# Kernel optimization log

Measured on AMD Instinct MI355X. Metric: run time of the kernel, lower is better.

Reference implementation:

```python
import jax, jax.numpy as jnp
import numpy as np

N, E, T = 6144, 98304, 32
D_IN, D, D_FF, H, OUT = 128, 256, 256, 4, 2
DH = D // H
EPS = 1e-5


def setup_inputs() -> dict:
    key = jax.random.key(0)
    ks = jax.random.split(key, 24)
    s = 0.05
    inp = {
        "x": jax.random.normal(ks[0], (N, D_IN), jnp.float32),
        "edge_index": jax.random.randint(ks[1], (2, E), 0, N, jnp.int64 if jax.config.jax_enable_x64 else jnp.int32),
        "timesteps": jnp.sort(jax.random.randint(ks[2], (N,), 0, T)),
        "lin_l_w": jax.random.normal(ks[3], (D, D_IN), jnp.float32) * s,
        "lin_l_b": jnp.zeros((D,), jnp.float32),
        "lin_r_w": jax.random.normal(ks[4], (D, D_IN), jnp.float32) * s,
        "bn_gamma": jnp.ones((D,), jnp.float32),
        "bn_beta": jnp.zeros((D,), jnp.float32),
        "in_proj_w": jax.random.normal(ks[5], (2, 3 * D, D), jnp.float32) * s,
        "in_proj_b": jnp.zeros((2, 3 * D), jnp.float32),
        "out_w": jax.random.normal(ks[6], (2, D, D), jnp.float32) * s,
        "out_b": jnp.zeros((2, D), jnp.float32),
        "ff1_w": jax.random.normal(ks[7], (2, D_FF, D), jnp.float32) * s,
        "ff1_b": jnp.zeros((2, D_FF), jnp.float32),
        "ff2_w": jax.random.normal(ks[8], (2, D, D_FF), jnp.float32) * s,
        "ff2_b": jnp.zeros((2, D), jnp.float32),
        "ln1_g": jnp.ones((2, D), jnp.float32),
        "ln1_b": jnp.zeros((2, D), jnp.float32),
        "ln2_g": jnp.ones((2, D), jnp.float32),
        "ln2_b": jnp.zeros((2, D), jnp.float32),
        "cls_w": jax.random.normal(ks[9], (OUT, D), jnp.float32) * s,
        "cls_b": jnp.zeros((OUT,), jnp.float32),
    }
    return inp


def _layernorm(h, g, b):
    mu = jnp.mean(h, -1, keepdims=True)
    v = jnp.var(h, -1, keepdims=True)
    return (h - mu) * jax.lax.rsqrt(v + EPS) * g + b


def _forward(x, edge_index, timesteps, lin_l_w, lin_l_b, lin_r_w, bn_gamma, bn_beta,
             in_proj_w, in_proj_b, out_w, out_b, ff1_w, ff1_b, ff2_w, ff2_b,
             ln1_g, ln1_b, ln2_g, ln2_b, cls_w, cls_b):
    # SAGEConv (mean aggregation): out = lin_l(mean_{j->i} x_j) + lin_r(x_i)
    src, dst = edge_index[0], edge_index[1]
    agg = jax.ops.segment_sum(x[src], dst, num_segments=N)
    cnt = jax.ops.segment_sum(jnp.ones((E,), x.dtype), dst, num_segments=N)
    agg = agg / jnp.maximum(cnt, 1.0)[:, None]
    h = agg @ lin_l_w.T + lin_l_b + x @ lin_r_w.T

    # BatchNorm1d (training batch stats) + ReLU
    mu = jnp.mean(h, 0)
    var = jnp.var(h, 0)
    h = (h - mu) * jax.lax.rsqrt(var + EPS) * bn_gamma + bn_beta
    h = jax.nn.relu(h)

    # Per-timestep transformer == full attention with block-diagonal mask
    mask = timesteps[:, None] == timesteps[None, :]  # [N, N]
    neg = jnp.finfo(h.dtype).min

    for l in range(2):
        # self-attention (post-norm TransformerEncoderLayer)
        qkv = h @ in_proj_w[l].T + in_proj_b[l]             # [N, 3D]
        q, k, v = jnp.split(qkv, 3, axis=-1)
        q = q.reshape(N, H, DH).transpose(1, 0, 2)          # [H, N, DH]
        k = k.reshape(N, H, DH).transpose(1, 0, 2)
        v = v.reshape(N, H, DH).transpose(1, 0, 2)
        scores = jnp.einsum('hnd,hmd->hnm', q, k) / jnp.sqrt(jnp.asarray(DH, h.dtype))
        scores = jnp.where(mask[None], scores, neg)
        attn = jax.nn.softmax(scores, axis=-1)
        o = jnp.einsum('hnm,hmd->hnd', attn, v).transpose(1, 0, 2).reshape(N, D)
        o = o @ out_w[l].T + out_b[l]
        h = _layernorm(h + o, ln1_g[l], ln1_b[l])
        # FFN
        f = jax.nn.relu(h @ ff1_w[l].T + ff1_b[l]) @ ff2_w[l].T + ff2_b[l]
        h = _layernorm(h + f, ln2_g[l], ln2_b[l])

    return h @ cls_w.T + cls_b  # [N, OUT]


def reference(x, edge_index, timesteps, lin_l_w, lin_l_b, lin_r_w, bn_gamma, bn_beta,
              in_proj_w, in_proj_b, out_w, out_b, ff1_w, ff1_b, ff2_w, ff2_b,
              ln1_g, ln1_b, ln2_g, ln2_b, cls_w, cls_b):
    return _forward(x, edge_index, timesteps, lin_l_w, lin_l_b, lin_r_w, bn_gamma, bn_beta,
                    in_proj_w, in_proj_b, out_w, out_b, ff1_w, ff1_b, ff2_w, ff2_b,
                    ln1_g, ln1_b, ln2_g, ln2_b, cls_w, cls_b)
```

## Files before the change

kernel.cpp:

```cpp
#include <hip/hip_runtime.h>

#define NN   6144
#define EE   98304
#define DIN  128
#define DD   256
#define TT   32
#define NH   4
#define ATTN_Z 6
#define WROWS 3328

typedef __attribute__((ext_vector_type(8))) short short8;
typedef __attribute__((ext_vector_type(4))) float f32x4;
typedef unsigned short u16;

__device__ __forceinline__ float bf2f(u16 u) {
    return __uint_as_float(((unsigned)u) << 16);
}
__device__ __forceinline__ u16 f2bf(float f) {
    unsigned u = __float_as_uint(f);
    return (u16)((u + 0x7fffu + ((u >> 16) & 1u)) >> 16);
}
__device__ __forceinline__ unsigned pk2(float a, float b) {
    return (unsigned)f2bf(a) | ((unsigned)f2bf(b) << 16);
}
__device__ __forceinline__ float bnrelu(float v, float s, float q, float g, float b) {
    float mu = s * (1.0f / NN);
    float var = q * (1.0f / NN) - mu * mu;
    return fmaxf((v - mu) * rsqrtf(var + 1e-5f) * g + b, 0.0f);
}

__global__ void aml_hist_k(const int* __restrict__ ei, int* __restrict__ deg) {
    int e = blockIdx.x * 256 + threadIdx.x;
    if (e < EE) atomicAdd(&deg[ei[EE + e]], 1);
}

__global__ void aml_scan_k(const int* __restrict__ deg, int* __restrict__ rowptr,
                           int* __restrict__ cursor) {
    int t = threadIdx.x;
    int base = t * 24;
    int loc[24];
    int s = 0;
    #pragma unroll
    for (int j = 0; j < 24; ++j) { loc[j] = s; s += deg[base + j]; }
    __shared__ int part[256];
    part[t] = s;
    __syncthreads();
    for (int o = 1; o < 256; o <<= 1) {
        int v = (t >= o) ? part[t - o] : 0;
        __syncthreads();
        part[t] += v;
        __syncthreads();
    }
    int off = (t > 0) ? part[t - 1] : 0;
    #pragma unroll
    for (int j = 0; j < 24; ++j) {
        rowptr[base + j] = off + loc[j];
        cursor[base + j] = off + loc[j];
    }
    if (t == 255) rowptr[NN] = part[255];
}

__global__ void aml_scatter2_k(const int* __restrict__ ei, int* __restrict__ cursor,
                               int* __restrict__ eid) {
    int e = blockIdx.x * 256 + threadIdx.x;
    if (e >= EE) return;
    int slot = atomicAdd(&cursor[ei[EE + e]], 1);
    eid[slot] = ei[e];
}

__global__ void aml_gather_k(const float* __restrict__ x, const int* __restrict__ rowptr,
                             const int* __restrict__ eid, u16* __restrict__ ac) {
    int node = blockIdx.x * 4 + (threadIdx.x >> 6);
    int lane = threadIdx.x & 63;
    int p0 = rowptr[node], p1 = rowptr[node + 1];
    float ax = 0.f, ay = 0.f;
    int j = p0;
    for (; j + 1 < p1; j += 2) {
        int s0 = eid[j], s1 = eid[j + 1];
        float2 v0 = *(const float2*)(x + (size_t)s0 * DIN + lane * 2);
        float2 v1 = *(const float2*)(x + (size_t)s1 * DIN + lane * 2);
        ax += v0.x + v1.x; ay += v0.y + v1.y;
    }
    if (j < p1) {
        float2 v = *(const float2*)(x + (size_t)eid[j] * DIN + lane * 2);
        ax += v.x; ay += v.y;
    }
    float inv = 1.0f / fmaxf((float)(p1 - p0), 1.0f);
    float2 xr = *(const float2*)(x + (size_t)node * DIN + lane * 2);
    *(unsigned*)(ac + (size_t)node * DD + lane * 2) = pk2(ax * inv, ay * inv);
    *(unsigned*)(ac + (size_t)node * DD + DIN + lane * 2) = pk2(xr.x, xr.y);
}

__global__ void aml_prep_k(const float* __restrict__ lin_l_w, const float* __restrict__ lin_r_w,
                           const float* __restrict__ inp_w, const float* __restrict__ out_w,
                           const float* __restrict__ ff1_w, const float* __restrict__ ff2_w,
                           const int* __restrict__ ts, u16* __restrict__ wb,
                           int* __restrict__ offs) {
    int r = blockIdx.x;
    if (r == WROWS) {
        int t = threadIdx.x;
        if (t <= TT) {
            int lo = 0, hi = NN;
            while (lo < hi) { int mid = (lo + hi) >> 1; if (ts[mid] < t) lo = mid + 1; else hi = mid; }
            offs[t] = lo;
        }
        return;
    }
    int k = threadIdx.x;
    float v;
    if (r < 256) {
        v = (k < DIN) ? lin_l_w[r * DIN + k] : lin_r_w[r * DIN + (k - DIN)];
    } else {
        int r2 = r - 256;
        int l = r2 / 1536, r3 = r2 % 1536;
        const float* src; int rr;
        if (r3 < 768)       { src = inp_w + (size_t)l * 768 * DD; rr = r3; }
        else if (r3 < 1024) { src = out_w + (size_t)l * DD * DD;  rr = r3 - 768; }
        else if (r3 < 1280) { src = ff1_w + (size_t)l * DD * DD;  rr = r3 - 1024; }
        else                { src = ff2_w + (size_t)l * DD * DD;  rr = r3 - 1280; }
        v = src[(size_t)rr * DD + k];
    }
    wb[(size_t)r * DD + k] = f2bf(v);
}

template <int RELU, int AF32, int CF32, int BNSTAT, int BNAPPLY>
__global__ __launch_bounds__(256)
void aml_gemm_k(const void* __restrict__ A, const u16* __restrict__ Wb,
                const float* __restrict__ bias, void* __restrict__ C, int M,
                float* __restrict__ stats, const float* __restrict__ bng,
                const float* __restrict__ bnb, float* __restrict__ h2) {
    __shared__ __align__(16) unsigned char lds[65536];
    const int t = threadIdx.x;
    const int brow = blockIdx.x * 64;
    const int bcol = blockIdx.y * 64;

    const u16* srcW = Wb + (size_t)bcol * 256;
    #pragma unroll
    for (int p = 0; p < 8; ++p) {
        int c = t + p * 256;
        int row = c >> 5;
        int colb = (c & 31) * 16;
        int dst = row * 512 + (colb ^ ((row & 7) << 4));
        if (AF32) {
            const float* sA = (const float*)A + (size_t)(brow + row) * 256 + (c & 31) * 8;
            float4 a0 = *(const float4*)sA;
            float4 a1 = *(const float4*)(sA + 4);
            if (BNAPPLY) {
                int d0 = (c & 31) * 8;
                float4 s0 = *(const float4*)(stats + d0);
                float4 s1 = *(const float4*)(stats + d0 + 4);
                float4 q0 = *(const float4*)(stats + DD + d0);
                float4 q1 = *(const float4*)(stats + DD + d0 + 4);
                float4 g0 = *(const float4*)(bng + d0), g1 = *(const float4*)(bng + d0 + 4);
                float4 b0 = *(const float4*)(bnb + d0), b1 = *(const float4*)(bnb + d0 + 4);
                a0.x = bnrelu(a0.x, s0.x, q0.x, g0.x, b0.x);
                a0.y = bnrelu(a0.y, s0.y, q0.y, g0.y, b0.y);
                a0.z = bnrelu(a0.z, s0.z, q0.z, g0.z, b0.z);
                a0.w = bnrelu(a0.w, s0.w, q0.w, g0.w, b0.w);
                a1.x = bnrelu(a1.x, s1.x, q1.x, g1.x, b1.x);
                a1.y = bnrelu(a1.y, s1.y, q1.y, g1.y, b1.y);
                a1.z = bnrelu(a1.z, s1.z, q1.z, g1.z, b1.z);
                a1.w = bnrelu(a1.w, s1.w, q1.w, g1.w, b1.w);
                if (blockIdx.y == 0) {
                    float* hp = h2 + (size_t)(brow + row) * 256 + d0;
                    *(float4*)hp = a0;
                    *(float4*)(hp + 4) = a1;
                }
            }
            uint4 pa = { pk2(a0.x, a0.y), pk2(a0.z, a0.w), pk2(a1.x, a1.y), pk2(a1.z, a1.w) };
            *(uint4*)(lds + dst) = pa;
        } else {
            const u16* sA = (const u16*)A + (size_t)(brow + row) * 256 + (c & 31) * 8;
            *(uint4*)(lds + dst) = *(const uint4*)sA;
        }
        *(uint4*)(lds + 32768 + dst) = *(const uint4*)(srcW + (size_t)row * 256 + (c & 31) * 8);
    }
    __syncthreads();

    const int wave = t >> 6, lane = t & 63;
    const int lrow = lane & 15, lk = lane >> 4;
    const int arow = wave * 16 + lrow;
    f32x4 acc[4] = {};
    #pragma unroll
    for (int ks = 0; ks < 8; ++ks) {
        int kbyte = ks * 64 + lk * 16;
        short8 af = *(const short8*)(lds + arow * 512 + (kbyte ^ ((arow & 7) << 4)));
        #pragma unroll
        for (int ct = 0; ct < 4; ++ct) {
            int wrow = ct * 16 + lrow;
            short8 bf = *(const short8*)(lds + 32768 + wrow * 512 + (kbyte ^ ((wrow & 7) << 4)));
            acc[ct] = __builtin_amdgcn_mfma_f32_16x16x32_bf16(af, bf, acc[ct], 0, 0, 0);
        }
    }

    #pragma unroll
    for (int ct = 0; ct < 4; ++ct) {
        int col = bcol + ct * 16 + lrow;
        float bv = bias[col];
        float s = 0.f, q = 0.f;
        #pragma unroll
        for (int r = 0; r < 4; ++r) {
            int grow = brow + wave * 16 + lk * 4 + r;
            float v = acc[ct][r] + bv;
            if (RELU) v = fmaxf(v, 0.0f);
            if (CF32) ((float*)C)[(size_t)grow * M + col] = v;
            else      ((u16*)C)[(size_t)grow * M + col] = f2bf(v);
            if (BNSTAT) { s += v; q += v * v; }
        }
        if (BNSTAT) {
            s += __shfl_xor(s, 16); s += __shfl_xor(s, 32);
            q += __shfl_xor(q, 16); q += __shfl_xor(q, 32);
            if (lk == 0) {
                atomicAdd(&stats[col], s);
                atomicAdd(&stats[DD + col], q);
            }
        }
    }
}

template <int CLS>
__global__ __launch_bounds__(256)
void aml_mega_k(const u16* __restrict__ A, const u16* __restrict__ Wb,
                const float* __restrict__ bias, float* __restrict__ h,
                const float* __restrict__ g, const float* __restrict__ bv,
                const float* __restrict__ cls_w, const float* __restrict__ cls_b,
                float* __restrict__ out) {
    __shared__ __align__(16) unsigned char Al[8192];
    __shared__ __align__(16) unsigned char Wl[32768];
    __shared__ float reds[4][16], redq[4][16];
    __shared__ float redc[2][4][16];
    const int t = threadIdx.x;
    const int brow = blockIdx.x * 16;
    const int wave = t >> 6, lane = t & 63;
    const int lrow = lane & 15, lk = lane >> 4;
    const int wcol = wave * 64;

    #pragma unroll
    for (int p = 0; p < 2; ++p) {
        int c = t + p * 256;
        int row = c >> 5;
        int c8 = c & 31;
        const u16* sA = A + (size_t)(brow + row) * 256 + c8 * 8;
        *(uint4*)(Al + row * 512 + ((c8 * 16) ^ ((row & 7) << 4))) = *(const uint4*)sA;
    }

    short8 af[8];
    f32x4 acc[4] = {};
    for (int kc = 0; kc < 4; ++kc) {
        if (kc) __syncthreads();
        #pragma unroll
        for (int p = 0; p < 8; ++p) {
            int c = t + p * 256;
            int row = c >> 3, sub = c & 7;
            *(uint4*)(Wl + row * 128 + ((sub * 16) ^ ((row & 7) << 4))) =
                *(const uint4*)(Wb + (size_t)row * 256 + kc * 64 + sub * 8);
        }
        __syncthreads();
        if (kc == 0) {
            #pragma unroll
            for (int ks = 0; ks < 8; ++ks) {
                int kbyte = ks * 64 + lk * 16;
                af[ks] = *(const short8*)(Al + lrow * 512 + (kbyte ^ ((lrow & 7) << 4)));
            }
        }
        #pragma unroll
        for (int s = 0; s < 2; ++s) {
            int kb = s * 64 + lk * 16;
            #pragma unroll
            for (int ct = 0; ct < 4; ++ct) {
                int wrow = wcol + ct * 16 + lrow;
                short8 bf = *(const short8*)(Wl + wrow * 128 + (kb ^ ((wrow & 7) << 4)));
                acc[ct] = __builtin_amdgcn_mfma_f32_16x16x32_bf16(af[kc * 2 + s], bf, acc[ct], 0, 0, 0);
            }
        }
    }

    float s4[4] = {}, q4[4] = {};
    #pragma unroll
    for (int ct = 0; ct < 4; ++ct) {
        int col = wcol + ct * 16 + lrow;
        float bvv = bias[col];
        #pragma unroll
        for (int r = 0; r < 4; ++r) {
            int grow = brow + lk * 4 + r;
            float v = acc[ct][r] + bvv + h[(size_t)grow * DD + col];
            acc[ct][r] = v;
            s4[r] += v; q4[r] += v * v;
        }
    }
    #pragma unroll
    for (int off = 1; off < 16; off <<= 1) {
        #pragma unroll
        for (int r = 0; r < 4; ++r) {
            s4[r] += __shfl_xor(s4[r], off);
            q4[r] += __shfl_xor(q4[r], off);
        }
    }
    if (lrow == 0) {
        #pragma unroll
        for (int r = 0; r < 4; ++r) {
            reds[wave][lk * 4 + r] = s4[r];
            redq[wave][lk * 4 + r] = q4[r];
        }
    }
    __syncthreads();
    float mu[4], iv[4];
    #pragma unroll
    for (int r = 0; r < 4; ++r) {
        int rr = lk * 4 + r;
        float S = reds[0][rr] + reds[1][rr] + reds[2][rr] + reds[3][rr];
        float Q = redq[0][rr] + redq[1][rr] + redq[2][rr] + redq[3][rr];
        mu[r] = S * (1.0f / DD);
        iv[r] = rsqrtf(Q * (1.0f / DD) - mu[r] * mu[r] + 1e-5f);
    }
    float c0[4] = {}, c1[4] = {};
    #pragma unroll
    for (int ct = 0; ct < 4; ++ct) {
        int col = wcol + ct * 16 + lrow;
        float gv = g[col], bb = bv[col];
        float w0 = CLS ? cls_w[col] : 0.f;
        float w1 = CLS ? cls_w[DD + col] : 0.f;
        #pragma unroll
        for (int r = 0; r < 4; ++r) {
            int grow = brow + lk * 4 + r;
            float v = (acc[ct][r] - mu[r]) * iv[r] * gv + bb;
            h[(size_t)grow * DD + col] = v;
            if (CLS) { c0[r] += v * w0; c1[r] += v * w1; }
        }
    }
    if (CLS) {
        #pragma unroll
        for (int off = 1; off < 16; off <<= 1) {
            #pragma unroll
            for (int r = 0; r < 4; ++r) {
                c0[r] += __shfl_xor(c0[r], off);
                c1[r] += __shfl_xor(c1[r], off);
            }
        }
        if (lrow == 0) {
            #pragma unroll
            for (int r = 0; r < 4; ++r) {
                redc[0][wave][lk * 4 + r] = c0[r];
                redc[1][wave][lk * 4 + r] = c1[r];
            }
        }
        __syncthreads();
        if (wave == 0 && lrow == 0) {
            float cb0 = cls_b[0], cb1 = cls_b[1];
            #pragma unroll
            for (int r = 0; r < 4; ++r) {
                int rr = lk * 4 + r;
                float o0 = redc[0][0][rr] + redc[0][1][rr] + redc[0][2][rr] + redc[0][3][rr];
                float o1 = redc[1][0][rr] + redc[1][1][rr] + redc[1][2][rr] + redc[1][3][rr];
                out[(brow + rr) * 2]     = o0 + cb0;
                out[(brow + rr) * 2 + 1] = o1 + cb1;
            }
        }
    }
}

__global__ __launch_bounds__(256)
void aml_attn_k(const u16* __restrict__ qkv, const int* __restrict__ offs,
                u16* __restrict__ o) {
    int tb = blockIdx.x, head = blockIdx.y, z = blockIdx.z;
    int start = offs[tb], end = offs[tb + 1];
    int S = end - start;
    if (S <= z * 64) return;
    int t = threadIdx.x, wave = t >> 6, lane = t & 63;
    int lq = lane & 15, lk = lane >> 4;
    int qoff = head * 64;

    __shared__ __align__(16) unsigned char Kl[8192];
    __shared__ __align__(16) unsigned char Vt[8192];
    __shared__ __align__(16) unsigned char Pl[4][2048];
    __shared__ float Ol[4][16][65];

    int qi = start + z * 64 + wave * 16 + lq;
    int qic = min(qi, end - 1);
    const u16* qp = qkv + (size_t)qic * 768 + qoff + lk * 8;
    short8 qf[2];
    qf[0] = *(const short8*)qp;
    qf[1] = *(const short8*)(qp + 32);

    float m = -1e30f, l = 0.f;
    f32x4 acc[4] = {};

    int ntile = (S + 63) >> 6;
    for (int tile = 0; tile < ntile; ++tile) {
        int jcnt = S - tile * 64; if (jcnt > 64) jcnt = 64;
        {
            int j = t >> 2, d0 = (t & 3) * 16;
            unsigned char* krow = Kl + j * 128;
            if (j < jcnt) {
                const u16* kp = qkv + (size_t)(start + tile * 64 + j) * 768 + 256 + qoff + d0;
                *(uint4*)(krow + ((d0 * 2) ^ ((j & 7) << 4))) = *(const uint4*)kp;
                *(uint4*)(krow + ((d0 * 2 + 16) ^ ((j & 7) << 4))) = *(const uint4*)(kp + 8);
                const u16* vp = kp + 256;
                #pragma unroll
                for (int i = 0; i < 16; ++i) {
                    int d = d0 + i;
                    *(u16*)(Vt + d * 128 + ((j * 2) ^ ((d & 7) << 4))) = vp[i];
                }
            } else {
                uint4 zz = { 0, 0, 0, 0 };
                *(uint4*)(krow + ((d0 * 2) ^ ((j & 7) << 4))) = zz;
                *(uint4*)(krow + ((d0 * 2 + 16) ^ ((j & 7) << 4))) = zz;
                #pragma unroll
                for (int i = 0; i < 16; ++i) {
                    int d = d0 + i;
                    *(u16*)(Vt + d * 128 + ((j * 2) ^ ((d & 7) << 4))) = 0;
                }
            }
        }
        __syncthreads();

        f32x4 sv[4];
        #pragma unroll
        for (int kt = 0; kt < 4; ++kt) {
            int kr = kt * 16 + lq;
            f32x4 s = {};
            #pragma unroll
            for (int ks = 0; ks < 2; ++ks) {
                short8 kf = *(const short8*)(Kl + kr * 128 + ((ks * 64 + lk * 16) ^ ((kr & 7) << 4)));
                s = __builtin_amdgcn_mfma_f32_16x16x32_bf16(kf, qf[ks], s, 0, 0, 0);
            }
            sv[kt] = s;
        }
        float pm = -1e30f;
        #pragma unroll
        for (int kt = 0; kt < 4; ++kt) {
            #pragma unroll
            for (int r = 0; r < 4; ++r) {
                int kk = tile * 64 + kt * 16 + lk * 4 + r;
                float s = (kk < S) ? sv[kt][r] * 0.125f : -1e30f;
                sv[kt][r] = s;
                pm = fmaxf(pm, s);
            }
        }
        pm = fmaxf(pm, __shfl_xor(pm, 16));
        pm = fmaxf(pm, __shfl_xor(pm, 32));
        float mn = fmaxf(m, pm);
        float corr = __expf(m - mn);
        m = mn;
        float ps = 0.f;
        #pragma unroll
        for (int kt = 0; kt < 4; ++kt) {
            #pragma unroll
            for (int r = 0; r < 4; ++r) {
                float p = __expf(sv[kt][r] - mn);
                sv[kt][r] = p;
                ps += p;
            }
            uint2 w = { pk2(sv[kt][0], sv[kt][1]), pk2(sv[kt][2], sv[kt][3]) };
            *(uint2*)(Pl[wave] + lq * 128 + ((kt * 32 + lk * 8) ^ ((lq & 7) << 4))) = w;
        }
        ps += __shfl_xor(ps, 16);
        ps += __shfl_xor(ps, 32);
        l = l * corr + ps;
        #pragma unroll
        for (int dt = 0; dt < 4; ++dt) {
            #pragma unroll
            for (int r = 0; r < 4; ++r) acc[dt][r] *= corr;
        }
        #pragma unroll
        for (int ks = 0; ks < 2; ++ks) {
            short8 pf = *(const short8*)(Pl[wave] + lq * 128 + ((ks * 64 + lk * 16) ^ ((lq & 7) << 4)));
            #pragma unroll
            for (int dt = 0; dt < 4; ++dt) {
                int dr = dt * 16 + lq;
                short8 vf = *(const short8*)(Vt + dr * 128 + ((ks * 64 + lk * 16) ^ ((dr & 7) << 4)));
                acc[dt] = __builtin_amdgcn_mfma_f32_16x16x32_bf16(vf, pf, acc[dt], 0, 0, 0);
            }
        }
        __syncthreads();
    }

    float linv = 1.0f / l;
    #pragma unroll
    for (int dt = 0; dt < 4; ++dt) {
        #pragma unroll
        for (int r = 0; r < 4; ++r)
            Ol[wave][lq][dt * 16 + lk * 4 + r] = acc[dt][r] * linv;
    }
    int q2 = lane >> 2, c2 = lane & 3;
    int qg = start + z * 64 + wave * 16 + q2;
    if (qg < end) {
        u16* op = o + (size_t)qg * DD + qoff + c2 * 16;
        const float* sp = &Ol[wave][q2][c2 * 16];
        #pragma unroll
        for (int i = 0; i < 8; ++i)
            ((unsigned*)op)[i] = pk2(sp[2 * i], sp[2 * i + 1]);
    }
}

extern "C" void kernel_launch(void* const* d_in, const int* in_sizes, int n_in,
                              void* d_out, int out_size, void* d_ws, size_t ws_size,
                              hipStream_t stream) {
    const float* x       = (const float*)d_in[0];
    const int*   ei      = (const int*)d_in[1];
    const int*   ts      = (const int*)d_in[2];
    const float* lin_l_w = (const float*)d_in[3];
    const float* lin_l_b = (const float*)d_in[4];
    const float* lin_r_w = (const float*)d_in[5];
    const float* bn_g    = (const float*)d_in[6];
    const float* bn_b    = (const float*)d_in[7];
    const float* inp_w   = (const float*)d_in[8];
    const float* inp_b   = (const float*)d_in[9];
    const float* out_w   = (const float*)d_in[10];
    const float* out_b   = (const float*)d_in[11];
    const float* ff1_w   = (const float*)d_in[12];
    const float* ff1_b   = (const float*)d_in[13];
    const float* ff2_w   = (const float*)d_in[14];
    const float* ff2_b   = (const float*)d_in[15];
    const float* ln1_g   = (const float*)d_in[16];
    const float* ln1_b   = (const float*)d_in[17];
    const float* ln2_g   = (const float*)d_in[18];
    const float* ln2_b   = (const float*)d_in[19];
    const float* cls_w   = (const float*)d_in[20];
    const float* cls_b   = (const float*)d_in[21];

    float* ws     = (float*)d_ws;
    float* stats  = ws;
    int*   deg    = (int*)(stats + 512);
    int*   rowptr = deg + NN;
    int*   cursor = rowptr + NN + 4;
    int*   eid    = cursor + NN;
    int*   offs   = eid + EE;
    u16*   wb     = (u16*)(offs + 64);
    float* h      = (float*)(wb + (size_t)WROWS * 256);
    float* h2     = h + (size_t)NN * DD;
    u16*   qkv    = (u16*)(h2 + (size_t)NN * DD);
    u16*   t1     = qkv + (size_t)NN * 768;
    u16*   ac     = qkv;

    const u16* wb_cat = wb;
    const u16* wb_inp[2] = { wb + (size_t)(256) * 256,        wb + (size_t)(256 + 1536) * 256 };
    const u16* wb_out[2] = { wb + (size_t)(256 + 768) * 256,  wb + (size_t)(256 + 1536 + 768) * 256 };
    const u16* wb_ff1[2] = { wb + (size_t)(256 + 1024) * 256, wb + (size_t)(256 + 1536 + 1024) * 256 };
    const u16* wb_ff2[2] = { wb + (size_t)(256 + 1280) * 256, wb + (size_t)(256 + 1536 + 1280) * 256 };

    hipMemsetAsync(stats, 0, 512 * sizeof(float) + NN * sizeof(int), stream);

    aml_hist_k<<<EE / 256, 256, 0, stream>>>(ei, deg);
    aml_scan_k<<<1, 256, 0, stream>>>(deg, rowptr, cursor);
    aml_scatter2_k<<<EE / 256, 256, 0, stream>>>(ei, cursor, eid);
    aml_gather_k<<<NN / 4, 256, 0, stream>>>(x, rowptr, eid, ac);
    aml_prep_k<<<WROWS + 1, 256, 0, stream>>>(lin_l_w, lin_r_w, inp_w, out_w, ff1_w, ff2_w,
                                              ts, wb, offs);
    aml_gemm_k<0, 0, 1, 1, 0><<<dim3(NN / 64, 4), 256, 0, stream>>>(
        ac, wb_cat, lin_l_b, h, DD, stats, nullptr, nullptr, nullptr);

    for (int l = 0; l < 2; ++l) {
        if (l == 0)
            aml_gemm_k<0, 1, 0, 0, 1><<<dim3(NN / 64, 12), 256, 0, stream>>>(
                h, wb_inp[0], inp_b, qkv, 768, stats, bn_g, bn_b, h2);
        else
            aml_gemm_k<0, 1, 0, 0, 0><<<dim3(NN / 64, 12), 256, 0, stream>>>(
                h2, wb_inp[1], inp_b + 768, qkv, 768, nullptr, nullptr, nullptr, nullptr);
        aml_attn_k<<<dim3(TT, NH, ATTN_Z), 256, 0, stream>>>(qkv, offs, t1);
        aml_mega_k<0><<<NN / 16, 256, 0, stream>>>(t1, wb_out[l], out_b + (size_t)l * DD, h2,
                                                   ln1_g + (size_t)l * DD, ln1_b + (size_t)l * DD,
                                                   nullptr, nullptr, nullptr);
        aml_gemm_k<1, 1, 0, 0, 0><<<dim3(NN / 64, 4), 256, 0, stream>>>(
            h2, wb_ff1[l], ff1_b + (size_t)l * DD, t1, DD, nullptr, nullptr, nullptr, nullptr);
        if (l == 0)
            aml_mega_k<0><<<NN / 16, 256, 0, stream>>>(t1, wb_ff2[0], ff2_b, h2,
                                                       ln2_g, ln2_b, nullptr, nullptr, nullptr);
        else
            aml_mega_k<1><<<NN / 16, 256, 0, stream>>>(t1, wb_ff2[1], ff2_b + DD, h2,
                                                       ln2_g + DD, ln2_b + DD,
                                                       cls_w, cls_b, (float*)d_out);
    }
}
```

Before: 162.5 us.

## Use bf16 activation copies and 128-column GEMM tiles reusing A fragments

Mega kernels now write a bf16 copy of the residual stream alongside the fp32 one, and the following GEMMs read that bf16 copy instead of converting fp32 on load. The SAGE GEMM writes bf16 output, and the BN+ReLU step is applied while loading that bf16 input. Each GEMM block now covers two 64-column weight tiles, keeping A fragments in registers and reloading only W, which halves the grid and the redundant A loads. The memset is replaced by a small zero kernel. The cost is extra bf16 stores, extra syncs inside the GEMM, and an added rounding step before BN.

```diff
diff --git a/kernel.cpp b/kernel.cpp
--- a/kernel.cpp
+++ b/kernel.cpp
@@ -27,6 +27,10 @@
     float mu = s * (1.0f / NN);
     float var = q * (1.0f / NN) - mu * mu;
     return fmaxf((v - mu) * rsqrtf(var + 1e-5f) * g + b, 0.0f);
+}
+
+__global__ void aml_zero_k(float* __restrict__ p) {
+    p[blockIdx.x * 256 + threadIdx.x] = 0.0f;
 }
 
 __global__ void aml_hist_k(const int* __restrict__ ei, int* __restrict__ deg) {
@@ -123,7 +127,7 @@
     wb[(size_t)r * DD + k] = f2bf(v);
 }
 
-template <int RELU, int AF32, int CF32, int BNSTAT, int BNAPPLY>
+template <int RELU, int AMODE, int CF32, int BNSTAT, int CT2>
 __global__ __launch_bounds__(256)
 void aml_gemm_k(const void* __restrict__ A, const u16* __restrict__ Wb,
                 const float* __restrict__ bias, void* __restrict__ C, int M,
@@ -132,87 +136,109 @@
     __shared__ __align__(16) unsigned char lds[65536];
     const int t = threadIdx.x;
     const int brow = blockIdx.x * 64;
-    const int bcol = blockIdx.y * 64;
-
-    const u16* srcW = Wb + (size_t)bcol * 256;
+    const int bcol = blockIdx.y * (64 * CT2);
+
     #pragma unroll
     for (int p = 0; p < 8; ++p) {
         int c = t + p * 256;
         int row = c >> 5;
         int colb = (c & 31) * 16;
         int dst = row * 512 + (colb ^ ((row & 7) << 4));
-        if (AF32) {
+        if (AMODE == 1) {
             const float* sA = (const float*)A + (size_t)(brow + row) * 256 + (c & 31) * 8;
             float4 a0 = *(const float4*)sA;
             float4 a1 = *(const float4*)(sA + 4);
-            if (BNAPPLY) {
-                int d0 = (c & 31) * 8;
-                float4 s0 = *(const float4*)(stats + d0);
-                float4 s1 = *(const float4*)(stats + d0 + 4);
-                float4 q0 = *(const float4*)(stats + DD + d0);
-                float4 q1 = *(const float4*)(stats + DD + d0 + 4);
-                float4 g0 = *(const float4*)(bng + d0), g1 = *(const float4*)(bng + d0 + 4);
-                float4 b0 = *(const float4*)(bnb + d0), b1 = *(const float4*)(bnb + d0 + 4);
-                a0.x = bnrelu(a0.x, s0.x, q0.x, g0.x, b0.x);
-                a0.y = bnrelu(a0.y, s0.y, q0.y, g0.y, b0.y);
-                a0.z = bnrelu(a0.z, s0.z, q0.z, g0.z, b0.z);
-                a0.w = bnrelu(a0.w, s0.w, q0.w, g0.w, b0.w);
-                a1.x = bnrelu(a1.x, s1.x, q1.x, g1.x, b1.x);
-                a1.y = bnrelu(a1.y, s1.y, q1.y, g1.y, b1.y);
-                a1.z = bnrelu(a1.z, s1.z, q1.z, g1.z, b1.z);
-                a1.w = bnrelu(a1.w, s1.w, q1.w, g1.w, b1.w);
-                if (blockIdx.y == 0) {
-                    float* hp = h2 + (size_t)(brow + row) * 256 + d0;
-                    *(float4*)hp = a0;
-                    *(float4*)(hp + 4) = a1;
-                }
-            }
             uint4 pa = { pk2(a0.x, a0.y), pk2(a0.z, a0.w), pk2(a1.x, a1.y), pk2(a1.z, a1.w) };
+            *(uint4*)(lds + dst) = pa;
+        } else if (AMODE == 2) {
+            int d0 = (c & 31) * 8;
+            const u16* sA = (const u16*)A + (size_t)(brow + row) * 256 + d0;
+            uint4 raw = *(const uint4*)sA;
+            const u16* rp = (const u16*)&raw;
+            float av[8];
+            #pragma unroll
+            for (int i = 0; i < 8; ++i) {
+                int d = d0 + i;
+                av[i] = bnrelu(bf2f(rp[i]), stats[d], stats[DD + d], bng[d], bnb[d]);
+            }
+            if (blockIdx.y == 0) {
+                float* hp = h2 + (size_t)(brow + row) * 256 + d0;
+                *(float4*)hp = make_float4(av[0], av[1], av[2], av[3]);
+                *(float4*)(hp + 4) = make_float4(av[4], av[5], av[6], av[7]);
+            }
+            uint4 pa = { pk2(av[0], av[1]), pk2(av[2], av[3]), pk2(av[4], av[5]), pk2(av[6], av[7]) };
             *(uint4*)(lds + dst) = pa;
         } else {
             const u16* sA = (const u16*)A + (size_t)(brow + row) * 256 + (c & 31) * 8;
             *(uint4*)(lds + dst) = *(const uint4*)sA;
         }
-        *(uint4*)(lds + 32768 + dst) = *(const uint4*)(srcW + (size_t)row * 256 + (c & 31) * 8);
+        *(uint4*)(lds + 32768 + dst) =
+            *(const uint4*)(Wb + (size_t)(bcol + row) * 256 + (c & 31) * 8);
     }
     __syncthreads();
 
     const int wave = t >> 6, lane = t & 63;
     const int lrow = lane & 15, lk = lane >> 4;
     const int arow = wave * 16 + lrow;
-    f32x4 acc[4] = {};
+
+    short8 af[8];
     #pragma unroll
     for (int ks = 0; ks < 8; ++ks) {
         int kbyte = ks * 64 + lk * 16;
-        short8 af = *(const short8*)(lds + arow * 512 + (kbyte ^ ((arow & 7) << 4)));
+        af[ks] = *(const short8*)(lds + arow * 512 + (kbyte ^ ((arow & 7) << 4)));
+    }
+
+    f32x4 acc[CT2][4] = {};
+    #pragma unroll
+    for (int c2 = 0; c2 < CT2; ++c2) {
+        if (c2) {
+            __syncthreads();
+            #pragma unroll
+            for (int p = 0; p < 8; ++p) {
+                int c = t + p * 256;
+                int row = c >> 5;
+                int colb = (c & 31) * 16;
+                int dst = 32768 + row * 512 + (colb ^ ((row & 7) << 4));
+                *(uint4*)(lds + dst) =
+                    *(const uint4*)(Wb + (size_t)(bcol + c2 * 64 + row) * 256 + (c & 31) * 8);
+            }
+            __syncthreads();
+        }
+        #pragma unroll
+        for (int ks = 0; ks < 8; ++ks) {
+            int kbyte = ks * 64 + lk * 16;
+            #pragma unroll
+            for (int ct = 0; ct < 4; ++ct) {
+                int wrow = ct * 16 + lrow;
+                short8 bf = *(const short8*)(lds + 32768 + wrow * 512 + (kbyte ^ ((wrow & 7) << 4)));
+                acc[c2][ct] = __builtin_amdgcn_mfma_f32_16x16x32_bf16(af[ks], bf, acc[c2][ct], 0, 0, 0);
+            }
+        }
+    }
+
+    #pragma unroll
+    for (int c2 = 0; c2 < CT2; ++c2) {
         #pragma unroll
         for (int ct = 0; ct < 4; ++ct) {
-            int wrow = ct * 16 + lrow;
-            short8 bf = *(const short8*)(lds + 32768 + wrow * 512 + (kbyte ^ ((wrow & 7) << 4)));
-            acc[ct] = __builtin_amdgcn_mfma_f32_16x16x32_bf16(af, bf, acc[ct], 0, 0, 0);
-        }
-    }
-
-    #pragma unroll
-    for (int ct = 0; ct < 4; ++ct) {
-        int col = bcol + ct * 16 + lrow;
-        float bv = bias[col];
-        float s = 0.f, q = 0.f;
-        #pragma unroll
-        for (int r = 0; r < 4; ++r) {
-            int grow = brow + wave * 16 + lk * 4 + r;
-            float v = acc[ct][r] + bv;
-            if (RELU) v = fmaxf(v, 0.0f);
-            if (CF32) ((float*)C)[(size_t)grow * M + col] = v;
-            else      ((u16*)C)[(size_t)grow * M + col] = f2bf(v);
-            if (BNSTAT) { s += v; q += v * v; }
-        }
-        if (BNSTAT) {
-            s += __shfl_xor(s, 16); s += __shfl_xor(s, 32);
-            q += __shfl_xor(q, 16); q += __shfl_xor(q, 32);
-            if (lk == 0) {
-                atomicAdd(&stats[col], s);
-                atomicAdd(&stats[DD + col], q);
+            int col = bcol + c2 * 64 + ct * 16 + lrow;
+            float bv = bias[col];
+            float s = 0.f, q = 0.f;
+            #pragma unroll
+            for (int r = 0; r < 4; ++r) {
+                int grow = brow + wave * 16 + lk * 4 + r;
+                float v = acc[c2][ct][r] + bv;
+                if (RELU) v = fmaxf(v, 0.0f);
+                if (CF32) ((float*)C)[(size_t)grow * M + col] = v;
+                else      ((u16*)C)[(size_t)grow * M + col] = f2bf(v);
+                if (BNSTAT) { s += v; q += v * v; }
+            }
+            if (BNSTAT) {
+                s += __shfl_xor(s, 16); s += __shfl_xor(s, 32);
+                q += __shfl_xor(q, 16); q += __shfl_xor(q, 32);
+                if (lk == 0) {
+                    atomicAdd(&stats[col], s);
+                    atomicAdd(&stats[DD + col], q);
+                }
             }
         }
     }
@@ -222,6 +248,7 @@
 __global__ __launch_bounds__(256)
 void aml_mega_k(const u16* __restrict__ A, const u16* __restrict__ Wb,
                 const float* __restrict__ bias, float* __restrict__ h,
+                u16* __restrict__ h2b,
                 const float* __restrict__ g, const float* __restrict__ bv,
                 const float* __restrict__ cls_w, const float* __restrict__ cls_b,
                 float* __restrict__ out) {
@@ -325,6 +352,7 @@
             int grow = brow + lk * 4 + r;
             float v = (acc[ct][r] - mu[r]) * iv[r] * gv + bb;
             h[(size_t)grow * DD + col] = v;
+            h2b[(size_t)grow * DD + col] = f2bf(v);
             if (CLS) { c0[r] += v * w0; c1[r] += v * w1; }
         }
     }
@@ -527,9 +555,10 @@
     int*   eid    = cursor + NN;
     int*   offs   = eid + EE;
     u16*   wb     = (u16*)(offs + 64);
-    float* h      = (float*)(wb + (size_t)WROWS * 256);
-    float* h2     = h + (size_t)NN * DD;
-    u16*   qkv    = (u16*)(h2 + (size_t)NN * DD);
+    u16*   hb     = wb + (size_t)WROWS * 256;
+    float* h2     = (float*)(hb + (size_t)NN * DD);
+    u16*   h2b    = (u16*)(h2 + (size_t)NN * DD);
+    u16*   qkv    = h2b + (size_t)NN * DD;
     u16*   t1     = qkv + (size_t)NN * 768;
     u16*   ac     = qkv;
 
@@ -539,35 +568,34 @@
     const u16* wb_ff1[2] = { wb + (size_t)(256 + 1024) * 256, wb + (size_t)(256 + 1536 + 1024) * 256 };
     const u16* wb_ff2[2] = { wb + (size_t)(256 + 1280) * 256, wb + (size_t)(256 + 1536 + 1280) * 256 };
 
-    hipMemsetAsync(stats, 0, 512 * sizeof(float) + NN * sizeof(int), stream);
-
+    aml_zero_k<<<26, 256, 0, stream>>>(stats);
     aml_hist_k<<<EE / 256, 256, 0, stream>>>(ei, deg);
     aml_scan_k<<<1, 256, 0, stream>>>(deg, rowptr, cursor);
     aml_scatter2_k<<<EE / 256, 256, 0, stream>>>(ei, cursor, eid);
     aml_gather_k<<<NN / 4, 256, 0, stream>>>(x, rowptr, eid, ac);
     aml_prep_k<<<WROWS + 1, 256, 0, stream>>>(lin_l_w, lin_r_w, inp_w, out_w, ff1_w, ff2_w,
                                               ts, wb, offs);
-    aml_gemm_k<0, 0, 1, 1, 0><<<dim3(NN / 64, 4), 256, 0, stream>>>(
-        ac, wb_cat, lin_l_b, h, DD, stats, nullptr, nullptr, nullptr);
+    aml_gemm_k<0, 0, 0, 1, 2><<<dim3(NN / 64, 2), 256, 0, stream>>>(
+        ac, wb_cat, lin_l_b, hb, DD, stats, nullptr, nullptr, nullptr);
 
     for (int l = 0; l < 2; ++l) {
         if (l == 0)
-            aml_gemm_k<0, 1, 0, 0, 1><<<dim3(NN / 64, 12), 256, 0, stream>>>(
-                h, wb_inp[0], inp_b, qkv, 768, stats, bn_g, bn_b, h2);
+            aml_gemm_k<0, 2, 0, 0, 2><<<dim3(NN / 64, 6), 256, 0, stream>>>(
+                hb, wb_inp[0], inp_b, qkv, 768, stats, bn_g, bn_b, h2);
         else
-            aml_gemm_k<0, 1, 0, 0, 0><<<dim3(NN / 64, 12), 256, 0, stream>>>(
-                h2, wb_inp[1], inp_b + 768, qkv, 768, nullptr, nullptr, nullptr, nullptr);
+            aml_gemm_k<0, 0, 0, 0, 2><<<dim3(NN / 64, 6), 256, 0, stream>>>(
+                h2b, wb_inp[1], inp_b + 768, qkv, 768, nullptr, nullptr, nullptr, nullptr);
         aml_attn_k<<<dim3(TT, NH, ATTN_Z), 256, 0, stream>>>(qkv, offs, t1);
-        aml_mega_k<0><<<NN / 16, 256, 0, stream>>>(t1, wb_out[l], out_b + (size_t)l * DD, h2,
+        aml_mega_k<0><<<NN / 16, 256, 0, stream>>>(t1, wb_out[l], out_b + (size_t)l * DD, h2, h2b,
                                                    ln1_g + (size_t)l * DD, ln1_b + (size_t)l * DD,
                                                    nullptr, nullptr, nullptr);
-        aml_gemm_k<1, 1, 0, 0, 0><<<dim3(NN / 64, 4), 256, 0, stream>>>(
-            h2, wb_ff1[l], ff1_b + (size_t)l * DD, t1, DD, nullptr, nullptr, nullptr, nullptr);
+        aml_gemm_k<1, 0, 0, 0, 2><<<dim3(NN / 64, 2), 256, 0, stream>>>(
+            h2b, wb_ff1[l], ff1_b + (size_t)l * DD, t1, DD, nullptr, nullptr, nullptr, nullptr);
         if (l == 0)
-            aml_mega_k<0><<<NN / 16, 256, 0, stream>>>(t1, wb_ff2[0], ff2_b, h2,
+            aml_mega_k<0><<<NN / 16, 256, 0, stream>>>(t1, wb_ff2[0], ff2_b, h2, h2b,
                                                        ln2_g, ln2_b, nullptr, nullptr, nullptr);
         else
-            aml_mega_k<1><<<NN / 16, 256, 0, stream>>>(t1, wb_ff2[1], ff2_b + DD, h2,
+            aml_mega_k<1><<<NN / 16, 256, 0, stream>>>(t1, wb_ff2[1], ff2_b + DD, h2, h2b,
                                                        ln2_g + DD, ln2_b + DD,
                                                        cls_w, cls_b, (float*)d_out);
     }
```

After: 166.6 us. +2.5%, slower.
